# Performance work log

Measured on AMD Instinct MI355X. Metric: run time of the kernel, lower is better.

The kernel has to match this reference:

```python
import jax, jax.numpy as jnp
import numpy as np
from jax import lax

STRIDE = 1
DILATION = 1


def setup_inputs() -> dict:
    key = jax.random.key(0)
    k1, k2 = jax.random.split(key)
    inp = jax.random.normal(k1, (16, 1, 512, 512), dtype=jnp.float32)   # [B, 1, H, W]
    weight = jax.random.normal(k2, (16, 32, 9, 9), dtype=jnp.float32)   # [B, J, k, k]
    return {"input": inp, "weight": weight}


def reference(input, weight):
    # Original: for each (batch i, out-channel j), conv2d(input[i:i+1], weight[i,j][None,None]).
    # Equivalent fused form: grouped conv with groups = B, one 1-channel group per sample.
    B, J, kh, kw = weight.shape
    _, Cin, H, W = input.shape  # Cin == 1 (required by the per-slice conv math)
    pad = kw // 2 - 1  # self.padding == 0 -> int(k/2) - 1 rule in forward
    x = input.reshape(1, B * Cin, H, W)           # [1, B, H, W]
    w = weight.reshape(B * J, 1, kh, kw)          # [B*J, 1, k, k]
    out = lax.conv_general_dilated(
        x, w,
        window_strides=(STRIDE, STRIDE),
        padding=[(pad, pad), (pad, pad)],
        rhs_dilation=(DILATION, DILATION),
        feature_group_count=B,
        dimension_numbers=("NCHW", "OIHW", "NCHW"),
    )  # [1, B*J, H', W']
    return out.reshape(B, J, out.shape[2], out.shape[3])
```

## Files before the change

### kernel.cpp

```cpp
#include <hip/hip_runtime.h>

#define BB  16
#define JJ  32
#define HH  512
#define WW  512
#define KK  9
#define PAD 3
#define OH  510
#define OW  510

#define RROWS  8
#define NRAW   16
#define IN_DW  268
#define IN_PITCH_B (IN_DW * 4)
#define IN_BYTES (NRAW * IN_PITCH_B)

#define D_PITCH 524
#define DBUF_OFF IN_BYTES
#define LDS_BYTES (DBUF_OFF + 16 * D_PITCH * 4)

#define WRAW_OFF DBUF_OFF

typedef __bf16 bf16x8 __attribute__((ext_vector_type(8)));
typedef float  f32x4  __attribute__((ext_vector_type(4)));

__device__ __forceinline__ unsigned pack2bf(float a, float b) {
    unsigned ua = __float_as_uint(a) + 0x8000u;
    unsigned ub = __float_as_uint(b) + 0x8000u;
    return (ua >> 16) | (ub & 0xFFFF0000u);
}

__device__ __forceinline__ void barrier_lds_only() {
    asm volatile("s_waitcnt lgkmcnt(0)" ::: "memory");
    __builtin_amdgcn_s_barrier();
}

__global__ __launch_bounds__(256, 3)
void conv_mfma_kernel(const float* __restrict__ in,
                      const float* __restrict__ wgt,
                      float* __restrict__ out) {
    __shared__ __align__(16) char lds[LDS_BYTES];

    const int tid  = threadIdx.x;
    const int lane = tid & 63;
    const int w    = tid >> 6;
    const int c    = lane & 15;
    const int q    = lane >> 4;
    const int g    = q >> 1;
    const int h    = q & 1;
    const int par  = w >> 1;

    const int id  = blockIdx.x;
    const int xcd = id & 7;
    const int wk  = xcd * 256 + (id >> 3);
    const int yt  = wk & 63;
    const int p   = wk >> 6;
    const int jg  = p & 1;
    const int bi  = p >> 1;
    const int y0  = yt * RROWS;

    {
        const uint4 z = make_uint4(0u, 0u, 0u, 0u);
        for (int idx = tid; idx < 800; idx += 256)
            *(uint4*)(lds + WRAW_OFF + idx * 16) = z;
    }
    __syncthreads();

    float* rawF = (float*)(lds + WRAW_OFF);
    const float* wB = wgt + (size_t)(bi * JJ + jg * 16) * (KK * KK);
    for (int idx = tid; idx < 16 * 81; idx += 256) {
        const int j   = idx / 81;
        const int rem = idx - j * 81;
        const int u   = rem / 9;
        const int v   = rem - u * 9;
        rawF[j * 200 + u * 20 + v + 1] = wB[idx];
    }
    __syncthreads();

    bf16x8 afrag[5];
    #pragma unroll
    for (int s = 0; s < 5; ++s) {
        const int u = 2 * s + g;
        const int base = c * 200 + u * 20 + 8 * h + par;
        float wv[8];
        #pragma unroll
        for (int e = 0; e < 8; ++e) wv[e] = rawF[base + e];
        const uint4 pk = make_uint4(pack2bf(wv[0], wv[1]), pack2bf(wv[2], wv[3]),
                                    pack2bf(wv[4], wv[5]), pack2bf(wv[6], wv[7]));
        afrag[s] = __builtin_bit_cast(bf16x8, pk);
    }

    const float* inB = in + (size_t)bi * (HH * WW);
    #pragma unroll 1
    for (int idx = tid; idx < NRAW * 66; idx += 256) {
        const int rr = idx / 66;
        const int m  = idx - rr * 66;
        const int gr = y0 - PAD + rr;
        float el[8];
        if ((unsigned)gr < (unsigned)HH) {
            const float* rp = inB + gr * WW + 8 * m - 4;
            if (m >= 1 && m <= 63) {
                const float4 a = *(const float4*)rp;
                const float4 b = *(const float4*)(rp + 4);
                el[0]=a.x; el[1]=a.y; el[2]=a.z; el[3]=a.w;
                el[4]=b.x; el[5]=b.y; el[6]=b.z; el[7]=b.w;
            } else {
                #pragma unroll
                for (int t = 0; t < 8; ++t) {
                    const int gx = 8 * m - 4 + t;
                    el[t] = ((unsigned)gx < (unsigned)WW) ? rp[t] : 0.f;
                }
            }
        } else {
            #pragma unroll
            for (int t = 0; t < 8; ++t) el[t] = 0.f;
        }
        *(uint4*)(lds + rr * IN_PITCH_B + m * 16) =
            make_uint4(pack2bf(el[0], el[1]), pack2bf(el[2], el[3]),
                       pack2bf(el[4], el[5]), pack2bf(el[6], el[7]));
    }
    __syncthreads();

    const uint* L = (const uint*)lds;
    const int dwl = c + par + 4 * h + 128 * (w & 1);
    float* D = (float*)(lds + DBUF_OFF);
    const int xb = 256 * (w & 1) + 2 * c + par;
    const size_t plane = (size_t)OH * OW;
    float* outB = out + (size_t)(bi * JJ + jg * 16) * plane;

    #pragma unroll 1
    for (int r = 0; r < RROWS; ++r) {
        f32x4 acc[8];
        #pragma unroll
        for (int i = 0; i < 8; ++i) acc[i] = (f32x4){0.f, 0.f, 0.f, 0.f};

        #pragma unroll
        for (int s = 0; s < 5; ++s) {
            int u = 2 * s + g;
            if (u > 8) u = 0;
            const int rowdw = (r + u) * IN_DW + dwl;
            #pragma unroll
            for (int i = 0; i < 8; ++i) {
                const int d = rowdw + 16 * i;
                const uint4 bf = make_uint4(L[d], L[d + 1], L[d + 2], L[d + 3]);
                acc[i] = __builtin_amdgcn_mfma_f32_16x16x32_bf16(
                             afrag[s], __builtin_bit_cast(bf16x8, bf), acc[i], 0, 0, 0);
            }
        }

        #pragma unroll
        for (int i = 0; i < 8; ++i) {
            const int x = xb + 32 * i;
            #pragma unroll
            for (int rg = 0; rg < 4; ++rg)
                D[(q * 4 + rg) * D_PITCH + x] = acc[i][rg];
        }
        barrier_lds_only();

        const int y = y0 + r;
        if (y < OH) {
            #pragma unroll
            for (int jj = 0; jj < 4; ++jj) {
                const int jl = w * 4 + jj;
                float* op = outB + (size_t)jl * plane + (size_t)y * OW;
                #pragma unroll
                for (int seg = 0; seg < 4; ++seg) {
                    const int px = seg * 128 + 2 * lane;
                    if (px + 1 < OW)
                        *(float2*)(op + px) = *(const float2*)&D[jl * D_PITCH + px];
                }
            }
        }
        barrier_lds_only();
    }
}

extern "C" void kernel_launch(void* const* d_in, const int* in_sizes, int n_in,
                              void* d_out, int out_size, void* d_ws, size_t ws_size,
                              hipStream_t stream) {
    const float* inp = (const float*)d_in[0];
    const float* wgt = (const float*)d_in[1];
    float* out = (float*)d_out;

    conv_mfma_kernel<<<dim3(2048), 256, 0, stream>>>(inp, wgt, out);
}
```

Before: 141.5 us.

## Register-block two output rows per pass to share LDS input fragments

Restructures the per-row MFMA loop so each pass computes output rows ra and ra+2 together. Six B fragments are loaded from LDS per column tile and feed ten MFMAs, instead of ten fragment loads per row. The goal is to cut LDS read traffic, which is the main cost of feeding the MFMAs. In exchange the accumulator register footprint doubles, which may limit occupancy under the launch bounds, and the staged input tile grows by one row to cover the extra reach.

```diff
diff --git a/kernel.cpp b/kernel.cpp
--- a/kernel.cpp
+++ b/kernel.cpp
@@ -10,7 +10,7 @@
 #define OW  510
 
 #define RROWS  8
-#define NRAW   16
+#define NRAW   17
 #define IN_DW  268
 #define IN_PITCH_B (IN_DW * 4)
 #define IN_BYTES (NRAW * IN_PITCH_B)
@@ -129,49 +129,67 @@
     float* outB = out + (size_t)(bi * JJ + jg * 16) * plane;
 
     #pragma unroll 1
-    for (int r = 0; r < RROWS; ++r) {
-        f32x4 acc[8];
-        #pragma unroll
-        for (int i = 0; i < 8; ++i) acc[i] = (f32x4){0.f, 0.f, 0.f, 0.f};
-
-        #pragma unroll
-        for (int s = 0; s < 5; ++s) {
-            int u = 2 * s + g;
-            if (u > 8) u = 0;
-            const int rowdw = (r + u) * IN_DW + dwl;
+    for (int half = 0; half < 2; ++half) {
+        #pragma unroll 1
+        for (int pr = 0; pr < 2; ++pr) {
+            const int ra = half + 4 * pr;
+            f32x4 accA[8], accB[8];
             #pragma unroll
             for (int i = 0; i < 8; ++i) {
-                const int d = rowdw + 16 * i;
-                const uint4 bf = make_uint4(L[d], L[d + 1], L[d + 2], L[d + 3]);
-                acc[i] = __builtin_amdgcn_mfma_f32_16x16x32_bf16(
-                             afrag[s], __builtin_bit_cast(bf16x8, bf), acc[i], 0, 0, 0);
+                accA[i] = (f32x4){0.f, 0.f, 0.f, 0.f};
+                accB[i] = (f32x4){0.f, 0.f, 0.f, 0.f};
+            }
+
+            const int wbase = (ra + g) * IN_DW + dwl;
+            #pragma unroll
+            for (int i = 0; i < 8; ++i) {
+                uint4 F[6];
+                #pragma unroll
+                for (int t = 0; t < 6; ++t) {
+                    const int d = wbase + 2 * t * IN_DW + 16 * i;
+                    F[t] = make_uint4(L[d], L[d + 1], L[d + 2], L[d + 3]);
+                }
+                #pragma unroll
+                for (int s = 0; s < 5; ++s) {
+                    accA[i] = __builtin_amdgcn_mfma_f32_16x16x32_bf16(
+                                  afrag[s], __builtin_bit_cast(bf16x8, F[s]),
+                                  accA[i], 0, 0, 0);
+                    accB[i] = __builtin_amdgcn_mfma_f32_16x16x32_bf16(
+                                  afrag[s], __builtin_bit_cast(bf16x8, F[s + 1]),
+                                  accB[i], 0, 0, 0);
+                }
+            }
+
+            #pragma unroll
+            for (int rb = 0; rb < 2; ++rb) {
+                #pragma unroll
+                for (int i = 0; i < 8; ++i) {
+                    const int x = xb + 32 * i;
+                    #pragma unroll
+                    for (int rg = 0; rg < 4; ++rg)
+                        D[(q * 4 + rg) * D_PITCH + x] =
+                            rb ? accB[i][rg] : accA[i][rg];
+                }
+                barrier_lds_only();
+
+                const int y = y0 + ra + 2 * rb;
+                if (y < OH) {
+                    #pragma unroll
+                    for (int jj = 0; jj < 4; ++jj) {
+                        const int jl = w * 4 + jj;
+                        float* op = outB + (size_t)jl * plane + (size_t)y * OW;
+                        #pragma unroll
+                        for (int seg = 0; seg < 4; ++seg) {
+                            const int px = seg * 128 + 2 * lane;
+                            if (px + 1 < OW)
+                                *(float2*)(op + px) =
+                                    *(const float2*)&D[jl * D_PITCH + px];
+                        }
+                    }
+                }
+                barrier_lds_only();
             }
         }
-
-        #pragma unroll
-        for (int i = 0; i < 8; ++i) {
-            const int x = xb + 32 * i;
-            #pragma unroll
-            for (int rg = 0; rg < 4; ++rg)
-                D[(q * 4 + rg) * D_PITCH + x] = acc[i][rg];
-        }
-        barrier_lds_only();
-
-        const int y = y0 + r;
-        if (y < OH) {
-            #pragma unroll
-            for (int jj = 0; jj < 4; ++jj) {
-                const int jl = w * 4 + jj;
-                float* op = outB + (size_t)jl * plane + (size_t)y * OW;
-                #pragma unroll
-                for (int seg = 0; seg < 4; ++seg) {
-                    const int px = seg * 128 + 2 * lane;
-                    if (px + 1 < OW)
-                        *(float2*)(op + px) = *(const float2*)&D[jl * D_PITCH + px];
-                }
-            }
-        }
-        barrier_lds_only();
     }
 }
 
```

Result: slower. 159.2 us (+12.5%).
